# Optimization experiments

Measured on AMD Instinct MI355X. Metric: run time of the kernel, lower is better.

## Reference

```python
import jax, jax.numpy as jnp
import numpy as np

VOCAB, H, MAXLEN = 50257, 1024, 128


def setup_inputs() -> dict:
    key = jax.random.key(0)
    ks = jax.random.split(key, 14)
    s = 0.02  # init scale
    f32 = jnp.float32
    return {
        "x": jax.random.randint(ks[0], (1,), 0, VOCAB),
        "h": jax.random.normal(ks[1], (1, 1, H), f32),
        "encoder_outputs": jax.random.normal(ks[2], (MAXLEN, H), f32),
        "emb": jax.random.normal(ks[3], (VOCAB, H), f32) * s,
        "W_attn": jax.random.normal(ks[4], (MAXLEN, 2 * H), f32) * s,
        "b_attn": jnp.zeros((MAXLEN,), f32),
        "W_comb": jax.random.normal(ks[5], (H, 2 * H), f32) * s,
        "b_comb": jnp.zeros((H,), f32),
        "w_ih": jax.random.normal(ks[6], (3 * H, H), f32) * s,
        "w_hh": jax.random.normal(ks[7], (3 * H, H), f32) * s,
        "b_ih": jnp.zeros((3 * H,), f32),
        "b_hh": jnp.zeros((3 * H,), f32),
        "W_out": jax.random.normal(ks[8], (VOCAB, H), f32) * s,
        "b_out": jnp.zeros((VOCAB,), f32),
    }


def reference(x, h, encoder_outputs, emb, W_attn, b_attn, W_comb, b_comb,
              w_ih, w_hh, b_ih, b_hh, W_out, b_out):
    # Single decode step (batch=1, seq=1); dropout in eval mode (identity).
    e = emb[x]                       # [1, H] embedded token
    h0 = h[0]                        # [1, H] hidden state
    # attention over encoder outputs
    attn_w = jax.nn.softmax(jnp.concatenate([e, h0], axis=1) @ W_attn.T + b_attn, axis=1)  # [1, MAXLEN]
    attn_applied = attn_w @ encoder_outputs                                                 # [1, H]
    # combine + relu
    g = jax.nn.relu(jnp.concatenate([e, attn_applied], axis=1) @ W_comb.T + b_comb)        # [1, H]
    # single-step GRU (PyTorch gate order: r, z, n)
    gi = g @ w_ih.T + b_ih           # [1, 3H]
    gh = h0 @ w_hh.T + b_hh          # [1, 3H]
    i_r, i_z, i_n = jnp.split(gi, 3, axis=1)
    h_r, h_z, h_n = jnp.split(gh, 3, axis=1)
    r = jax.nn.sigmoid(i_r + h_r)
    z = jax.nn.sigmoid(i_z + h_z)
    n = jnp.tanh(i_n + r * h_n)
    h_new = (1.0 - z) * n + z * h0   # [1, H]
    out = jax.nn.log_softmax(h_new @ W_out.T + b_out, axis=1)  # [1, VOCAB]
    return out, h_new[None], attn_w
```

## Files before the change

### kernel.cpp

```cpp
#include <hip/hip_runtime.h>
#include <math.h>

#define H 1024
#define MAXLEN 128
#define VOCAB 50257

#define ROWS_PB 16
#define NB_OUT ((VOCAB + ROWS_PB - 1) / ROWS_PB)
#define NB_SUB ((VOCAB + 1023) / 1024)
#define NB_GH 768
#define NB_PRE (NB_GH + 32)

__device__ inline float wave_reduce_sum(float v) {
    #pragma unroll
    for (int off = 32; off > 0; off >>= 1) v += __shfl_down(v, off);
    return v;
}

__device__ inline float dot4(float4 a, float4 b) {
    return a.x * b.x + a.y * b.y + a.z * b.z + a.w * b.w;
}

__global__ void k_pre(const int* x, const float* h, const float* emb,
                      const float* W_attn, const float* b_attn,
                      const float* w_hh, const float* b_hh,
                      float* gh, float* logits) {
    const int lane = threadIdx.x & 63, wid = threadIdx.x >> 6;
    const float4* h4 = (const float4*)h;
    if (blockIdx.x < NB_GH) {
        int row = blockIdx.x * 4 + wid;
        const float4* w4 = (const float4*)(w_hh + (long long)row * H);
        float acc = 0.f;
        #pragma unroll
        for (int i = 0; i < 4; i++) {
            int idx = lane + i * 64;
            acc += dot4(w4[idx], h4[idx]);
        }
        acc = wave_reduce_sum(acc);
        if (lane == 0) gh[row] = acc + b_hh[row];
    } else {
        int row = (blockIdx.x - NB_GH) * 4 + wid;
        const float4* w4 = (const float4*)(W_attn + row * (2 * H));
        const float4* e4 = (const float4*)(emb + (long long)x[0] * H);
        float acc = 0.f;
        #pragma unroll
        for (int i = 0; i < 8; i++) {
            int idx = lane + i * 64;
            float4 wv = w4[idx];
            float4 cv = (idx < 256) ? e4[idx] : h4[idx - 256];
            acc += dot4(wv, cv);
        }
        acc = wave_reduce_sum(acc);
        if (lane == 0) logits[row] = acc + b_attn[row];
    }
}

__global__ void __launch_bounds__(1024, 1) k_sm_combine(
    const int* x, const float* emb, const float* logits,
    const float* enc, const float* W_comb, const float* b_comb,
    float* g_vec, float* out_attn) {
    __shared__ float buf[MAXLEN];
    __shared__ float wsm[MAXLEN];
    __shared__ float attn[H] __attribute__((aligned(16)));
    const int t = threadIdx.x;
    const int lane = t & 63, wid = t >> 6;

    if (t < MAXLEN) buf[t] = logits[t];
    __syncthreads();
    float m = -INFINITY;
    #pragma unroll 8
    for (int k = 0; k < MAXLEN; k++) m = fmaxf(m, buf[k]);
    if (t < MAXLEN) wsm[t] = expf(buf[t] - m);
    __syncthreads();
    float s = 0.f;
    #pragma unroll 8
    for (int k = 0; k < MAXLEN; k++) s += wsm[k];
    const float inv = 1.f / s;

    {
        float acc = 0.f;
        #pragma unroll 8
        for (int k = 0; k < MAXLEN; k++) acc += wsm[k] * enc[k * H + t];
        attn[t] = acc * inv;
    }
    if (blockIdx.x == 0 && t < MAXLEN) out_attn[t] = wsm[t] * inv;
    __syncthreads();

    if (wid < 4) {
        const int row = blockIdx.x * 4 + wid;
        const float4* w4 = (const float4*)(W_comb + (long long)row * (2 * H));
        const float4* e4 = (const float4*)(emb + (long long)x[0] * H);
        const float4* a4 = (const float4*)attn;
        float acc = 0.f;
        #pragma unroll
        for (int i = 0; i < 4; i++) {
            int idx = lane + i * 64;
            acc += dot4(w4[idx], e4[idx]);
        }
        #pragma unroll
        for (int i = 4; i < 8; i++) {
            int idx = lane + i * 64;
            acc += dot4(w4[idx], a4[idx - 256]);
        }
        acc = wave_reduce_sum(acc);
        if (lane == 0) g_vec[row] = fmaxf(acc + b_comb[row], 0.f);
    }
}

__global__ void k_gru(const float* g, const float* h, const float* gh,
                      const float* w_ih, const float* b_ih, float* h_new) {
    const int j = blockIdx.x, t = threadIdx.x;
    const int lane = t & 63, wid = t >> 6;
    __shared__ float red3[4][3];
    const float4* g4 = (const float4*)g;
    float4 vg = g4[t];
    float a3[3];
    #pragma unroll
    for (int gt = 0; gt < 3; gt++) {
        const float4* wi = (const float4*)(w_ih + (long long)(j + gt * H) * H);
        a3[gt] = dot4(wi[t], vg);
    }
    #pragma unroll
    for (int k = 0; k < 3; k++) {
        float v = a3[k];
        #pragma unroll
        for (int off = 32; off > 0; off >>= 1) v += __shfl_down(v, off);
        if (lane == 0) red3[wid][k] = v;
    }
    __syncthreads();
    if (t == 0) {
        float d[3];
        #pragma unroll
        for (int k = 0; k < 3; k++)
            d[k] = red3[0][k] + red3[1][k] + red3[2][k] + red3[3][k];
        float gi_r = d[0] + b_ih[j];
        float gi_z = d[1] + b_ih[j + H];
        float gi_n = d[2] + b_ih[j + 2 * H];
        float gh_r = gh[j];
        float gh_z = gh[j + H];
        float gh_n = gh[j + 2 * H];
        float r = 1.f / (1.f + expf(-(gi_r + gh_r)));
        float z = 1.f / (1.f + expf(-(gi_z + gh_z)));
        float n = tanhf(gi_n + r * gh_n);
        h_new[j] = (1.f - z) * n + z * h[j];
    }
}

__global__ void k_out_matvec(const float* hn, const float* W_out, const float* b_out,
                             float* out, float* pmax, float* psum) {
    const int t = threadIdx.x;
    const int lane = t & 63, wid = t >> 6;
    const int row0 = blockIdx.x * ROWS_PB + wid * 4;
    __shared__ float lm[ROWS_PB];

    const float4* h4 = (const float4*)hn;
    float4 hreg[4];
    #pragma unroll
    for (int i = 0; i < 4; i++) hreg[i] = h4[lane + i * 64];

    float lv[4] = {-INFINITY, -INFINITY, -INFINITY, -INFINITY};
    if (row0 + 3 < VOCAB) {
        float4 a[4][4];
        #pragma unroll
        for (int r = 0; r < 4; r++) {
            const float4* w4 = (const float4*)(W_out + (long long)(row0 + r) * H);
            #pragma unroll
            for (int i = 0; i < 4; i++) a[r][i] = w4[lane + i * 64];
        }
        #pragma unroll
        for (int r = 0; r < 4; r++) {
            float acc = 0.f;
            #pragma unroll
            for (int i = 0; i < 4; i++) acc += dot4(a[r][i], hreg[i]);
            acc = wave_reduce_sum(acc);
            if (lane == 0) {
                lv[r] = acc + b_out[row0 + r];
                out[row0 + r] = lv[r];
            }
        }
    } else {
        for (int r = 0; r < 4; r++) {
            int row = row0 + r;
            if (row >= VOCAB) break;
            const float4* w4 = (const float4*)(W_out + (long long)row * H);
            float acc = 0.f;
            #pragma unroll
            for (int i = 0; i < 4; i++) acc += dot4(w4[lane + i * 64], hreg[i]);
            acc = wave_reduce_sum(acc);
            if (lane == 0) {
                lv[r] = acc + b_out[row];
                out[row] = lv[r];
            }
        }
    }
    if (lane == 0) {
        #pragma unroll
        for (int r = 0; r < 4; r++) lm[wid * 4 + r] = lv[r];
    }
    __syncthreads();
    if (t == 0) {
        float m = -INFINITY;
        #pragma unroll
        for (int i = 0; i < ROWS_PB; i++) m = fmaxf(m, lm[i]);
        float s = 0.f;
        #pragma unroll
        for (int i = 0; i < ROWS_PB; i++)
            if (lm[i] != -INFINITY) s += expf(lm[i] - m);
        pmax[blockIdx.x] = m;
        psum[blockIdx.x] = s;
    }
}

__global__ void k_merge_sub(const float* pmax, const float* psum, float* out) {
    __shared__ float red[16];
    __shared__ float Msh;
    const int t = threadIdx.x;
    const int lane = t & 63, wid = t >> 6;
    float m = -INFINITY;
    for (int i = t; i < NB_OUT; i += 1024) m = fmaxf(m, pmax[i]);
    #pragma unroll
    for (int off = 32; off > 0; off >>= 1) m = fmaxf(m, __shfl_down(m, off));
    if (lane == 0) red[wid] = m;
    __syncthreads();
    if (t == 0) {
        float mm = red[0];
        #pragma unroll
        for (int i = 1; i < 16; i++) mm = fmaxf(mm, red[i]);
        Msh = mm;
    }
    __syncthreads();
    const float M = Msh;
    float s = 0.f;
    for (int i = t; i < NB_OUT; i += 1024) s += psum[i] * expf(pmax[i] - M);
    s = wave_reduce_sum(s);
    __syncthreads();
    if (lane == 0) red[wid] = s;
    __syncthreads();
    if (t == 0) {
        float ss = 0.f;
        #pragma unroll
        for (int i = 0; i < 16; i++) ss += red[i];
        Msh = M + logf(ss);
    }
    __syncthreads();
    const float c = Msh;
    int v = blockIdx.x * 1024 + t;
    if (v < VOCAB) out[v] -= c;
}

extern "C" void kernel_launch(void* const* d_in, const int* in_sizes, int n_in,
                              void* d_out, int out_size, void* d_ws, size_t ws_size,
                              hipStream_t stream) {
    const int*   x     = (const int*)d_in[0];
    const float* h     = (const float*)d_in[1];
    const float* enc   = (const float*)d_in[2];
    const float* emb   = (const float*)d_in[3];
    const float* W_attn= (const float*)d_in[4];
    const float* b_attn= (const float*)d_in[5];
    const float* W_comb= (const float*)d_in[6];
    const float* b_comb= (const float*)d_in[7];
    const float* w_ih  = (const float*)d_in[8];
    const float* w_hh  = (const float*)d_in[9];
    const float* b_ih  = (const float*)d_in[10];
    const float* b_hh  = (const float*)d_in[11];
    const float* W_out = (const float*)d_in[12];
    const float* b_out = (const float*)d_in[13];

    float* out      = (float*)d_out;
    float* out_h    = out + VOCAB;
    float* out_attn = out + VOCAB + H;

    float* ws          = (float*)d_ws;
    float* logits128   = ws;
    float* g_vec       = ws + 256;
    float* gh          = ws + 1536;
    float* pmax        = ws + 8192;
    float* psum        = ws + 16384;

    k_pre<<<NB_PRE, 256, 0, stream>>>(x, h, emb, W_attn, b_attn, w_hh, b_hh,
                                      gh, logits128);
    k_sm_combine<<<H / 4, 1024, 0, stream>>>(x, emb, logits128, enc,
                                             W_comb, b_comb, g_vec, out_attn);
    k_gru<<<H, 256, 0, stream>>>(g_vec, h, gh, w_ih, b_ih, out_h);
    k_out_matvec<<<NB_OUT, 256, 0, stream>>>(out_h, W_out, b_out, out, pmax, psum);
    k_merge_sub<<<NB_SUB, 1024, 0, stream>>>(pmax, psum, out);
}
```

Measured before the change: 70.39 us.

## Move attention softmax and context into k_pre, slim combine kernel

The attention logits, softmax and context vector (attn_applied) are now computed inside k_pre by 8 extra blocks. Each of those blocks recomputes all 128 attention logits redundantly and then produces a 128-column slice of the context. Previously each of 256 blocks of 1024 threads redid the softmax and the full 128x1024 context product before the W_comb matvec. The change removes that per-block redundant work, and k_combine becomes a light 256-thread matvec. The risk is a longer critical path in k_pre, since each of the 8 attention blocks serially computes 128 rows of dot products with only 4 waves.

```diff
diff --git a/kernel.cpp b/kernel.cpp
--- a/kernel.cpp
+++ b/kernel.cpp
@@ -9,7 +9,7 @@
 #define NB_OUT ((VOCAB + ROWS_PB - 1) / ROWS_PB)
 #define NB_SUB ((VOCAB + 1023) / 1024)
 #define NB_GH 768
-#define NB_PRE (NB_GH + 32)
+#define NB_PRE (NB_GH + 8)
 
 __device__ inline float wave_reduce_sum(float v) {
     #pragma unroll
@@ -23,9 +23,9 @@
 
 __global__ void k_pre(const int* x, const float* h, const float* emb,
                       const float* W_attn, const float* b_attn,
-                      const float* w_hh, const float* b_hh,
-                      float* gh, float* logits) {
-    const int lane = threadIdx.x & 63, wid = threadIdx.x >> 6;
+                      const float* w_hh, const float* b_hh, const float* enc,
+                      float* gh, float* attn_applied, float* out_attn) {
+    const int t = threadIdx.x, lane = t & 63, wid = t >> 6;
     const float4* h4 = (const float4*)h;
     if (blockIdx.x < NB_GH) {
         int row = blockIdx.x * 4 + wid;
@@ -39,72 +39,63 @@
         acc = wave_reduce_sum(acc);
         if (lane == 0) gh[row] = acc + b_hh[row];
     } else {
-        int row = (blockIdx.x - NB_GH) * 4 + wid;
-        const float4* w4 = (const float4*)(W_attn + row * (2 * H));
+        __shared__ float lg[MAXLEN];
+        __shared__ float wsm[MAXLEN];
         const float4* e4 = (const float4*)(emb + (long long)x[0] * H);
-        float acc = 0.f;
-        #pragma unroll
-        for (int i = 0; i < 8; i++) {
-            int idx = lane + i * 64;
-            float4 wv = w4[idx];
-            float4 cv = (idx < 256) ? e4[idx] : h4[idx - 256];
-            acc += dot4(wv, cv);
-        }
-        acc = wave_reduce_sum(acc);
-        if (lane == 0) logits[row] = acc + b_attn[row];
-    }
-}
-
-__global__ void __launch_bounds__(1024, 1) k_sm_combine(
-    const int* x, const float* emb, const float* logits,
-    const float* enc, const float* W_comb, const float* b_comb,
-    float* g_vec, float* out_attn) {
-    __shared__ float buf[MAXLEN];
-    __shared__ float wsm[MAXLEN];
-    __shared__ float attn[H] __attribute__((aligned(16)));
-    const int t = threadIdx.x;
-    const int lane = t & 63, wid = t >> 6;
-
-    if (t < MAXLEN) buf[t] = logits[t];
-    __syncthreads();
-    float m = -INFINITY;
-    #pragma unroll 8
-    for (int k = 0; k < MAXLEN; k++) m = fmaxf(m, buf[k]);
-    if (t < MAXLEN) wsm[t] = expf(buf[t] - m);
-    __syncthreads();
-    float s = 0.f;
-    #pragma unroll 8
-    for (int k = 0; k < MAXLEN; k++) s += wsm[k];
-    const float inv = 1.f / s;
-
-    {
-        float acc = 0.f;
+        #pragma unroll 2
+        for (int r = 0; r < 32; r++) {
+            int row = wid * 32 + r;
+            const float4* w4 = (const float4*)(W_attn + row * (2 * H));
+            float acc = 0.f;
+            #pragma unroll
+            for (int i = 0; i < 8; i++) {
+                int idx = lane + i * 64;
+                float4 wv = w4[idx];
+                float4 cv = (idx < 256) ? e4[idx] : h4[idx - 256];
+                acc += dot4(wv, cv);
+            }
+            acc = wave_reduce_sum(acc);
+            if (lane == 0) lg[row] = acc + b_attn[row];
+        }
+        __syncthreads();
+        float m = -INFINITY;
         #pragma unroll 8
-        for (int k = 0; k < MAXLEN; k++) acc += wsm[k] * enc[k * H + t];
-        attn[t] = acc * inv;
-    }
-    if (blockIdx.x == 0 && t < MAXLEN) out_attn[t] = wsm[t] * inv;
-    __syncthreads();
-
-    if (wid < 4) {
-        const int row = blockIdx.x * 4 + wid;
-        const float4* w4 = (const float4*)(W_comb + (long long)row * (2 * H));
-        const float4* e4 = (const float4*)(emb + (long long)x[0] * H);
-        const float4* a4 = (const float4*)attn;
-        float acc = 0.f;
-        #pragma unroll
-        for (int i = 0; i < 4; i++) {
-            int idx = lane + i * 64;
-            acc += dot4(w4[idx], e4[idx]);
-        }
-        #pragma unroll
-        for (int i = 4; i < 8; i++) {
-            int idx = lane + i * 64;
-            acc += dot4(w4[idx], a4[idx - 256]);
-        }
-        acc = wave_reduce_sum(acc);
-        if (lane == 0) g_vec[row] = fmaxf(acc + b_comb[row], 0.f);
-    }
+        for (int k = 0; k < MAXLEN; k++) m = fmaxf(m, lg[k]);
+        if (t < MAXLEN) wsm[t] = expf(lg[t] - m);
+        __syncthreads();
+        float s = 0.f;
+        #pragma unroll 8
+        for (int k = 0; k < MAXLEN; k++) s += wsm[k];
+        const float inv = 1.f / s;
+        const int b = blockIdx.x - NB_GH;
+        if (t < MAXLEN) {
+            int j = b * MAXLEN + t;
+            float acc = 0.f;
+            #pragma unroll 8
+            for (int k = 0; k < MAXLEN; k++) acc += wsm[k] * enc[k * H + j];
+            attn_applied[j] = acc * inv;
+            if (b == 0) out_attn[t] = wsm[t] * inv;
+        }
+    }
+}
+
+__global__ void k_combine(const int* x, const float* emb, const float* attn_applied,
+                          const float* W_comb, const float* b_comb, float* g) {
+    int wid = threadIdx.x >> 6, lane = threadIdx.x & 63;
+    int row = blockIdx.x * 4 + wid;
+    const float4* w4 = (const float4*)(W_comb + (long long)row * (2 * H));
+    const float4* e4 = (const float4*)(emb + (long long)x[0] * H);
+    const float4* a4 = (const float4*)attn_applied;
+    float acc = 0.f;
+    #pragma unroll
+    for (int i = 0; i < 8; i++) {
+        int idx = lane + i * 64;
+        float4 wv = w4[idx];
+        float4 cv = (idx < 256) ? e4[idx] : a4[idx - 256];
+        acc += dot4(wv, cv);
+    }
+    acc = wave_reduce_sum(acc);
+    if (lane == 0) g[row] = fmaxf(acc + b_comb[row], 0.f);
 }
 
 __global__ void k_gru(const float* g, const float* h, const float* gh,
@@ -271,16 +262,15 @@
     float* out_attn = out + VOCAB + H;
 
     float* ws          = (float*)d_ws;
-    float* logits128   = ws;
-    float* g_vec       = ws + 256;
-    float* gh          = ws + 1536;
+    float* attn_applied= ws;
+    float* g_vec       = ws + 1024;
+    float* gh          = ws + 2048;
     float* pmax        = ws + 8192;
     float* psum        = ws + 16384;
 
-    k_pre<<<NB_PRE, 256, 0, stream>>>(x, h, emb, W_attn, b_attn, w_hh, b_hh,
-                                      gh, logits128);
-    k_sm_combine<<<H / 4, 1024, 0, stream>>>(x, emb, logits128, enc,
-                                             W_comb, b_comb, g_vec, out_attn);
+    k_pre<<<NB_PRE, 256, 0, stream>>>(x, h, emb, W_attn, b_attn, w_hh, b_hh, enc,
+                                      gh, attn_applied, out_attn);
+    k_combine<<<H / 4, 256, 0, stream>>>(x, emb, attn_applied, W_comb, b_comb, g_vec);
     k_gru<<<H, 256, 0, stream>>>(g_vec, h, gh, w_ih, b_ih, out_h);
     k_out_matvec<<<NB_OUT, 256, 0, stream>>>(out_h, W_out, b_out, out, pmax, psum);
     k_merge_sub<<<NB_SUB, 1024, 0, stream>>>(pmax, psum, out);
```

Result: slower. 91.33 us (+29.7%).
